# Performance work log

Hardware: AMD Instinct MI355X
Metric: run time of the kernel (lower is better)

The kernel has to match this reference:

```python
import jax, jax.numpy as jnp
import numpy as np

HIDDEN = 4096
LATENT = 32768


def setup_inputs() -> dict:
    key = jax.random.key(0)
    k1, k2, k3, k4, k5 = jax.random.split(key, 5)
    x = jax.random.normal(k1, (2, 2048, HIDDEN), dtype=jnp.float32)
    # learned params (loaded from checkpoint in the original; random here)
    pre_bias = jax.random.normal(k2, (HIDDEN,), dtype=jnp.float32) * 0.02
    latent_bias = jax.random.normal(k3, (LATENT,), dtype=jnp.float32) * 0.02
    # nn.Linear weights: encoder.weight [latent, hidden], decoder.weight [hidden, latent]
    enc_w = jax.random.normal(k4, (LATENT, HIDDEN), dtype=jnp.float32) / np.sqrt(HIDDEN)
    dec_w = jax.random.normal(k5, (HIDDEN, LATENT), dtype=jnp.float32) / np.sqrt(LATENT)
    return {"x": x, "pre_bias": pre_bias, "latent_bias": latent_bias,
            "enc_w": enc_w, "dec_w": dec_w, "k": 64}


def reference(x, pre_bias, latent_bias, enc_w, dec_w, k):
    B, S, H = x.shape
    L = enc_w.shape[0]
    # pre_acts = encoder(x - pre_bias) + latent_bias
    pre_acts = jnp.einsum('bsh,lh->bsl', x - pre_bias, enc_w) + latent_bias
    # TopK sparsification: keep top-k values per token, zero elsewhere
    flat = pre_acts.reshape(B * S, L)
    vals, idx = jax.lax.top_k(flat, k)                       # [N,k]
    rows = jnp.arange(B * S)[:, None]                        # [N,1]
    latents = jnp.zeros_like(flat).at[rows, idx].set(vals).reshape(B, S, L)
    # x_hat = decoder(latents) + pre_bias
    x_hat = jnp.einsum('bsl,hl->bsh', latents, dec_w) + pre_bias
    return latents, x_hat
```

## Files before the change

### kernel.cpp

```cpp
#include <hip/hip_runtime.h>
#include <hip/hip_fp16.h>

typedef unsigned short u16;
typedef unsigned int u32;
using f32x4 = __attribute__((ext_vector_type(4))) float;
using bf16x8 = __attribute__((ext_vector_type(8))) short;
using u32x4 = __attribute__((ext_vector_type(4))) u32;

#define M_TOK 4096
#define HID   4096
#define LAT   32768
#define TOPK  64

#define BM 128
#define BN 256
#define BK 32
#define NT (HID / BK)
#define LCAP 2048
#define CAND_T0 2.0f
#define WBAND 0.0625f

__device__ __forceinline__ u16 f2bf(float f) {
  u32 u = __builtin_bit_cast(u32, f);
  u32 r = 0x7fffu + ((u >> 16) & 1u);
  return (u16)((u + r) >> 16);
}

__global__ __launch_bounds__(256) void k_xs(const float* __restrict__ x,
                                            const float* __restrict__ pb,
                                            u16* __restrict__ xs) {
  size_t i = ((size_t)blockIdx.x * 256 + threadIdx.x) * 4;
  if (i >= (size_t)M_TOK * HID) return;
  float4 xv = *(const float4*)(x + i);
  float4 bv = *(const float4*)(pb + (i & (HID - 1)));
  ushort4 o;
  o.x = f2bf(xv.x - bv.x); o.y = f2bf(xv.y - bv.y);
  o.z = f2bf(xv.z - bv.z); o.w = f2bf(xv.w - bv.w);
  *(ushort4*)(xs + i) = o;
}

__global__ __launch_bounds__(256) void k_conv(const float* __restrict__ src,
                                              u16* __restrict__ dst, size_t n4) {
  size_t i = (size_t)blockIdx.x * 256 + threadIdx.x;
  size_t stride = (size_t)gridDim.x * 256;
  for (; i < n4; i += stride) {
    float4 v = ((const float4*)src)[i];
    ushort4 o;
    o.x = f2bf(v.x); o.y = f2bf(v.y); o.z = f2bf(v.z); o.w = f2bf(v.w);
    ((ushort4*)dst)[i] = o;
  }
}

__global__ __launch_bounds__(512, 4) void k_gemm(const u16* __restrict__ A,
                                                 const u16* __restrict__ B,
                                                 const float* __restrict__ lbias,
                                                 float2* __restrict__ lists,
                                                 int* __restrict__ cnt) {
  __shared__ __align__(16) u16 Asm[3][64][64];
  __shared__ __align__(16) u16 Bsm[3][128][64];
  const int tid = threadIdx.x;
  const int lane = tid & 63;
  const int wave = tid >> 6;
  const int wm = wave >> 2;
  const int wn = wave & 3;

  const int bid = blockIdx.x;
  const int wg = (bid & 7) * 512 + (bid >> 3);
  const int bm = (wg & 31) * BM;
  const int bn = (wg >> 5) * BN;

  const int sp = tid >> 3, sslot = tid & 7;
  const int ss0 = sslot ^ (sp & 7);
  const int sr = sp * 2 + (ss0 >> 2);
  const int sc = (ss0 & 3) << 3;
  const int sp2 = sp + 64;
  const int ss02 = sslot ^ (sp2 & 7);
  const int sr2 = sp2 * 2 + (ss02 >> 2);
  const int sc2 = (ss02 & 3) << 3;

  auto stage = [&](int t, int buf) {
    __builtin_amdgcn_global_load_lds(
        (const __attribute__((address_space(1))) void*)(
            A + (size_t)(bm + sr) * HID + t * BK + sc),
        (__attribute__((address_space(3))) void*)(&Asm[buf][sp][sslot << 3]), 16, 0, 0);
    __builtin_amdgcn_global_load_lds(
        (const __attribute__((address_space(1))) void*)(
            B + (size_t)(bn + sr) * HID + t * BK + sc),
        (__attribute__((address_space(3))) void*)(&Bsm[buf][sp][sslot << 3]), 16, 0, 0);
    __builtin_amdgcn_global_load_lds(
        (const __attribute__((address_space(1))) void*)(
            B + (size_t)(bn + sr2) * HID + t * BK + sc2),
        (__attribute__((address_space(3))) void*)(&Bsm[buf][sp2][sslot << 3]), 16, 0, 0);
  };

  const int chunk = lane >> 4;
  auto readA = [&](int buf, int m) -> bf16x8 {
    int r = wm * 64 + m * 16 + (lane & 15);
    int p = r >> 1;
    int s = (((r & 1) << 2) + chunk) ^ (p & 7);
    u32 off = (u32)(uintptr_t)(__attribute__((address_space(3))) const void*)(&Asm[buf][p][s << 3]);
    u32x4 rv;
    asm volatile("ds_read_b128 %0, %1" : "=v"(rv) : "v"(off));
    return __builtin_bit_cast(bf16x8, rv);
  };
  auto readB = [&](int buf, int n) -> bf16x8 {
    int r = wn * 64 + n * 16 + (lane & 15);
    int p = r >> 1;
    int s = (((r & 1) << 2) + chunk) ^ (p & 7);
    u32 off = (u32)(uintptr_t)(__attribute__((address_space(3))) const void*)(&Bsm[buf][p][s << 3]);
    u32x4 rv;
    asm volatile("ds_read_b128 %0, %1" : "=v"(rv) : "v"(off));
    return __builtin_bit_cast(bf16x8, rv);
  };

  f32x4 acc[4][4] = {};

#define BARRIER() asm volatile("s_barrier" ::: "memory")
#define LGKM0() do { asm volatile("s_waitcnt lgkmcnt(0)"); \
                     __builtin_amdgcn_sched_barrier(0); } while (0)
#define VMCNT3() asm volatile("s_waitcnt vmcnt(3)" ::: "memory")
#define VMCNT0() asm volatile("s_waitcnt vmcnt(0)" ::: "memory")

  stage(0, 0); stage(1, 1);
  VMCNT3();
  BARRIER();

#pragma unroll 1
  for (int t = 0; t < NT; ++t) {
    const int buf = t - (t / 3) * 3;
    if (t + 2 < NT) stage(t + 2, (t + 2) - ((t + 2) / 3) * 3);
    bf16x8 a[4], bb[4];
#pragma unroll
    for (int m = 0; m < 4; ++m) a[m] = readA(buf, m);
#pragma unroll
    for (int n = 0; n < 4; ++n) bb[n] = readB(buf, n);
    LGKM0();
    __builtin_amdgcn_s_setprio(1);
#pragma unroll
    for (int m = 0; m < 4; ++m)
#pragma unroll
      for (int n = 0; n < 4; ++n)
        acc[m][n] = __builtin_amdgcn_mfma_f32_16x16x32_bf16(a[m], bb[n], acc[m][n], 0, 0, 0);
    __builtin_amdgcn_s_setprio(0);
    if (t + 2 < NT) VMCNT3(); else VMCNT0();
    BARRIER();
  }

#pragma unroll
  for (int n = 0; n < 4; ++n) {
    int col = bn + wn * 64 + n * 16 + (lane & 15);
    float lb = lbias[col];
#pragma unroll
    for (int m = 0; m < 4; ++m) {
      int row = bm + wm * 64 + m * 16 + ((lane >> 4) << 2);
#pragma unroll
      for (int j = 0; j < 4; ++j) {
        float v = acc[m][n][j] + lb;
        if (v >= CAND_T0) {
          int p = atomicAdd(&cnt[row + j], 1);
          if (p < LCAP)
            lists[(size_t)(row + j) * LCAP + p] =
                make_float2(v, __builtin_bit_cast(float, col));
        }
      }
    }
  }
#undef BARRIER
#undef LGKM0
#undef VMCNT3
#undef VMCNT0
}

__global__ __launch_bounds__(256) void k_topk(
    const float2* __restrict__ lists, const int* __restrict__ cnt,
    const float* __restrict__ x,
    const float* __restrict__ pb,
    const float* __restrict__ enc_w,
    const float* __restrict__ lbias,
    int* __restrict__ oidx, float* __restrict__ oval) {
  const int row = blockIdx.x;
  const int tid = threadIdx.x;
  const int lane = tid & 63, wave = tid >> 6;

  __shared__ int cnum, innum, selnum;
  __shared__ float s_m;
  __shared__ int lidx[LCAP];
  __shared__ float laf[LCAP];
  __shared__ int cidx[352];
  __shared__ double cref[352];
  __shared__ int fidx[64];
  __shared__ float fval[64];

  const int n = min(cnt[row], LCAP);
  if (tid == 0) { s_m = -1e30f; cnum = 0; innum = 0; selnum = 0; }
  for (int j = tid; j < n; j += 256) {
    float2 e = lists[(size_t)row * LCAP + j];
    laf[j] = e.x;
    lidx[j] = __builtin_bit_cast(int, e.y);
  }
  __syncthreads();

  for (int j = tid; j < n; j += 256) {
    float aj = laf[j]; int ij = lidx[j];
    int rank = 0;
    for (int i2 = 0; i2 < n; ++i2) {
      float ai = laf[i2];
      rank += (ai > aj) || (ai == aj && lidx[i2] < ij);
    }
    if (rank == 63) s_m = aj;
  }
  __syncthreads();
  float mf = s_m;

  for (int j = tid; j < n; j += 256) {
    float aa = laf[j];
    if (aa > mf + WBAND) {
      int p = atomicAdd(&innum, 1);
      if (p < 64) { fidx[p] = lidx[j]; fval[p] = aa; }
    } else if (aa >= mf - WBAND) {
      int p = atomicAdd(&cnum, 1);
      if (p < 352) cidx[p] = lidx[j];
    }
  }
  __syncthreads();
  int nin = min(innum, 64);
  int nu = min(cnum, 352);

  const float* xrow = x + (size_t)row * HID;
  for (int cc = wave; cc < nu; cc += 4) {
    const float* wrow = enc_w + (size_t)cidx[cc] * HID;
    double s = 0.0;
    for (int i = lane * 4; i < HID; i += 256) {
      float4 wv = *(const float4*)(wrow + i);
      float4 xv = *(const float4*)(xrow + i);
      float4 bv = *(const float4*)(pb + i);
      s += ((double)xv.x - (double)bv.x) * (double)wv.x;
      s += ((double)xv.y - (double)bv.y) * (double)wv.y;
      s += ((double)xv.z - (double)bv.z) * (double)wv.z;
      s += ((double)xv.w - (double)bv.w) * (double)wv.w;
    }
#pragma unroll
    for (int off = 32; off > 0; off >>= 1) s += __shfl_down(s, off);
    if (lane == 0) cref[cc] = s + (double)lbias[cidx[cc]];
  }
  __syncthreads();

  int need = 64 - nin;
  for (int j = tid; j < nu; j += 256) {
    double rj = cref[j]; int ij = cidx[j];
    int rank = 0;
    for (int i2 = 0; i2 < nu; ++i2) {
      double ri = cref[i2];
      rank += (ri > rj) || (ri == rj && cidx[i2] < ij);
    }
    if (rank < need) {
      int p = atomicAdd(&selnum, 1);
      if (nin + p < 64) { fidx[nin + p] = ij; fval[nin + p] = (float)rj; }
    }
  }
  __syncthreads();

  if (tid < 64) {
    int my = fidx[tid]; float v = fval[tid];
    int rank = 0;
#pragma unroll
    for (int i2 = 0; i2 < 64; ++i2) rank += (fidx[i2] < my);
    oidx[row * 64 + rank] = my;
    oval[row * 64 + rank] = v;
  }
}

__global__ __launch_bounds__(256) void k_trans(const float* __restrict__ dw,
                                               u16* __restrict__ dt) {
  __shared__ float tile[64][65];
  int l0 = blockIdx.x * 64;
  int h0 = blockIdx.y * 64;
  int tx = threadIdx.x & 15;
  int ty = threadIdx.x >> 4;
#pragma unroll
  for (int i = 0; i < 4; ++i) {
    int r = ty + i * 16;
    float4 v = *(const float4*)(dw + (size_t)(h0 + r) * LAT + l0 + tx * 4);
    tile[r][tx * 4 + 0] = v.x; tile[r][tx * 4 + 1] = v.y;
    tile[r][tx * 4 + 2] = v.z; tile[r][tx * 4 + 3] = v.w;
  }
  __syncthreads();
#pragma unroll
  for (int i = 0; i < 4; ++i) {
    int r = ty + i * 16;
    ushort4 o;
    o.x = f2bf(tile[tx * 4 + 0][r]);
    o.y = f2bf(tile[tx * 4 + 1][r]);
    o.z = f2bf(tile[tx * 4 + 2][r]);
    o.w = f2bf(tile[tx * 4 + 3][r]);
    *(ushort4*)(dt + (size_t)(l0 + r) * HID + h0 + tx * 4) = o;
  }
}

__global__ __launch_bounds__(256) void k_decode(
    const int* __restrict__ oidx, const float* __restrict__ oval,
    const u16* __restrict__ dt, const float* __restrict__ pb,
    float* __restrict__ xh) {
  const int n = blockIdx.x, tid = threadIdx.x;
  __shared__ int sidx[64];
  __shared__ float sval[64];
  if (tid < 64) { sidx[tid] = oidx[n * 64 + tid]; sval[tid] = oval[n * 64 + tid]; }
  __syncthreads();
  const int h0 = tid * 16;
  float acc[16];
#pragma unroll
  for (int q = 0; q < 4; ++q) {
    float4 b = *(const float4*)(pb + h0 + q * 4);
    acc[q * 4 + 0] = b.x; acc[q * 4 + 1] = b.y;
    acc[q * 4 + 2] = b.z; acc[q * 4 + 3] = b.w;
  }
  for (int j = 0; j < 64; ++j) {
    float v = sval[j];
    const uint4* w = (const uint4*)(dt + (size_t)sidx[j] * HID + h0);
    uint4 p0 = w[0], p1 = w[1];
    u32 u[8] = {p0.x, p0.y, p0.z, p0.w, p1.x, p1.y, p1.z, p1.w};
#pragma unroll
    for (int q = 0; q < 8; ++q) {
      float lo = __builtin_bit_cast(float, u[q] << 16);
      float hi = __builtin_bit_cast(float, u[q] & 0xffff0000u);
      acc[q * 2 + 0] = fmaf(v, lo, acc[q * 2 + 0]);
      acc[q * 2 + 1] = fmaf(v, hi, acc[q * 2 + 1]);
    }
  }
#pragma unroll
  for (int q = 0; q < 4; ++q) {
    float4 o;
    o.x = acc[q * 4 + 0]; o.y = acc[q * 4 + 1];
    o.z = acc[q * 4 + 2]; o.w = acc[q * 4 + 3];
    *(float4*)(xh + (size_t)n * HID + h0 + q * 4) = o;
  }
}

__global__ __launch_bounds__(256) void k_lat(const int* __restrict__ oidx,
                                             const float* __restrict__ oval,
                                             float* __restrict__ lat) {
  const int n = blockIdx.x, tid = threadIdx.x;
  __shared__ int sidx[64];
  __shared__ float sval[64];
  if (tid < 64) { sidx[tid] = oidx[n * 64 + tid]; sval[tid] = oval[n * 64 + tid]; }
  float* row = lat + (size_t)n * LAT;
  float4 z = {0.f, 0.f, 0.f, 0.f};
  for (int q = tid; q < LAT / 4; q += 256) *(float4*)(row + q * 4) = z;
  __syncthreads();
  if (tid < 64) row[sidx[tid]] = sval[tid];
}

extern "C" void kernel_launch(void* const* d_in, const int* in_sizes, int n_in,
                              void* d_out, int out_size, void* d_ws, size_t ws_size,
                              hipStream_t stream) {
  const float* x = (const float*)d_in[0];
  const float* pre_bias = (const float*)d_in[1];
  const float* latent_bias = (const float*)d_in[2];
  const float* enc_w = (const float*)d_in[3];
  const float* dec_w = (const float*)d_in[4];

  float* latents = (float*)d_out;
  float* xhat = latents + (size_t)M_TOK * LAT;

  u16* xs = (u16*)xhat;
  u16* encb = (u16*)latents;
  float2* lists = (float2*)((char*)d_out + (size_t)M_TOK * LAT * 2);
  u16* decT = (u16*)latents;
  int* cnt = (int*)d_ws;
  int* oidx = (int*)((char*)d_ws + M_TOK * 4);
  float* oval = (float*)((char*)d_ws + M_TOK * 4 + (size_t)M_TOK * TOPK * 4);

  hipMemsetAsync(cnt, 0, M_TOK * 4, stream);
  k_xs<<<(M_TOK * HID / 4 + 255) / 256, 256, 0, stream>>>(x, pre_bias, xs);
  k_conv<<<4096, 256, 0, stream>>>(enc_w, encb, (size_t)LAT * HID / 4);
  k_gemm<<<(M_TOK / BM) * (LAT / BN), 512, 0, stream>>>(xs, encb, latent_bias, lists, cnt);
  k_topk<<<M_TOK, 256, 0, stream>>>(lists, cnt, x, pre_bias, enc_w, latent_bias, oidx, oval);
  k_trans<<<dim3(LAT / 64, HID / 64), 256, 0, stream>>>(dec_w, decT);
  k_decode<<<M_TOK, 256, 0, stream>>>(oidx, oval, decT, pre_bias, xhat);
  k_lat<<<M_TOK, 256, 0, stream>>>(oidx, oval, latents);
}
```

Measured before the change: 2.487 ms.

## Store transposed decoder weights in FP8 and fuse input conversion kernels

The decoder weight copy made by the transpose kernel is now stored as 8-bit floats scaled by 64, using hardware pack and unpack builtins where available and a software encoder otherwise. The decode kernel gathers half as many bytes per selected latent row, and the value scale is folded into the top-k values. The x-minus-bias conversion and the encoder weight bf16 conversion are merged into one grid-stride kernel, saving a launch. The top-k rescoring band (WBAND) is narrowed. FP8 weights lower decoder accuracy, and the narrower band may change which candidates get refined.

```diff
diff --git a/kernel.cpp b/kernel.cpp
--- a/kernel.cpp
+++ b/kernel.cpp
@@ -1,6 +1,7 @@
 #include <hip/hip_runtime.h>
 #include <hip/hip_fp16.h>
 
+typedef unsigned char u8;
 typedef unsigned short u16;
 typedef unsigned int u32;
 using f32x4 = __attribute__((ext_vector_type(4))) float;
@@ -18,7 +19,15 @@
 #define NT (HID / BK)
 #define LCAP 2048
 #define CAND_T0 2.0f
-#define WBAND 0.0625f
+#define WBAND 0.03f
+
+#if __has_builtin(__builtin_amdgcn_cvt_pk_f32_fp8) && __has_builtin(__builtin_amdgcn_cvt_pk_fp8_f32)
+#define HW_FP8 1
+#define VSCALE (1.0f / 64.0f)
+#else
+#define HW_FP8 0
+#define VSCALE 4.0f
+#endif
 
 __device__ __forceinline__ u16 f2bf(float f) {
   u32 u = __builtin_bit_cast(u32, f);
@@ -26,28 +35,43 @@
   return (u16)((u + r) >> 16);
 }
 
-__global__ __launch_bounds__(256) void k_xs(const float* __restrict__ x,
-                                            const float* __restrict__ pb,
-                                            u16* __restrict__ xs) {
-  size_t i = ((size_t)blockIdx.x * 256 + threadIdx.x) * 4;
-  if (i >= (size_t)M_TOK * HID) return;
-  float4 xv = *(const float4*)(x + i);
-  float4 bv = *(const float4*)(pb + (i & (HID - 1)));
-  ushort4 o;
-  o.x = f2bf(xv.x - bv.x); o.y = f2bf(xv.y - bv.y);
-  o.z = f2bf(xv.z - bv.z); o.w = f2bf(xv.w - bv.w);
-  *(ushort4*)(xs + i) = o;
-}
-
-__global__ __launch_bounds__(256) void k_conv(const float* __restrict__ src,
-                                              u16* __restrict__ dst, size_t n4) {
+#if !HW_FP8
+__device__ __forceinline__ u8 enc_fp8(float w) {
+  _Float16 hf = (_Float16)(w * 64.0f);
+  u16 h = __builtin_bit_cast(u16, hf);
+  u16 s = (h >> 8) & 0x80;
+  u16 mag = h & 0x7fff;
+  if (mag < 0x2400) return (u8)s;
+  int eman = ((int)mag + 0x40 - 0x2000) >> 7;
+  if (eman > 0x7e) eman = 0x7e;
+  return (u8)(s | eman);
+}
+__device__ __forceinline__ float dec_fp8(u32 b) {
+  u16 h = (u16)(((b & 0x80u) << 8) | ((b & 0x7fu) << 7));
+  return (float)__builtin_bit_cast(_Float16, h);
+}
+#endif
+
+__global__ __launch_bounds__(256) void k_convx(const float* __restrict__ x,
+                                               const float* __restrict__ pb,
+                                               u16* __restrict__ xs,
+                                               const float* __restrict__ ew,
+                                               u16* __restrict__ encb) {
+  const size_t stride = (size_t)gridDim.x * 256;
   size_t i = (size_t)blockIdx.x * 256 + threadIdx.x;
-  size_t stride = (size_t)gridDim.x * 256;
-  for (; i < n4; i += stride) {
-    float4 v = ((const float4*)src)[i];
+  for (size_t q = i; q < (size_t)M_TOK * HID / 4; q += stride) {
+    float4 xv = ((const float4*)x)[q];
+    float4 bv = *(const float4*)(pb + ((q * 4) & (HID - 1)));
+    ushort4 o;
+    o.x = f2bf(xv.x - bv.x); o.y = f2bf(xv.y - bv.y);
+    o.z = f2bf(xv.z - bv.z); o.w = f2bf(xv.w - bv.w);
+    ((ushort4*)xs)[q] = o;
+  }
+  for (size_t q = i; q < (size_t)LAT * HID / 4; q += stride) {
+    float4 v = ((const float4*)ew)[q];
     ushort4 o;
     o.x = f2bf(v.x); o.y = f2bf(v.y); o.z = f2bf(v.z); o.w = f2bf(v.w);
-    ((ushort4*)dst)[i] = o;
+    ((ushort4*)encb)[q] = o;
   }
 }
 
@@ -271,7 +295,7 @@
 }
 
 __global__ __launch_bounds__(256) void k_trans(const float* __restrict__ dw,
-                                               u16* __restrict__ dt) {
+                                               u8* __restrict__ dt) {
   __shared__ float tile[64][65];
   int l0 = blockIdx.x * 64;
   int h0 = blockIdx.y * 64;
@@ -288,23 +312,31 @@
 #pragma unroll
   for (int i = 0; i < 4; ++i) {
     int r = ty + i * 16;
-    ushort4 o;
-    o.x = f2bf(tile[tx * 4 + 0][r]);
-    o.y = f2bf(tile[tx * 4 + 1][r]);
-    o.z = f2bf(tile[tx * 4 + 2][r]);
-    o.w = f2bf(tile[tx * 4 + 3][r]);
-    *(ushort4*)(dt + (size_t)(l0 + r) * HID + h0 + tx * 4) = o;
+    float a = tile[tx * 4 + 0][r], b = tile[tx * 4 + 1][r];
+    float c = tile[tx * 4 + 2][r], d = tile[tx * 4 + 3][r];
+#if HW_FP8
+    int pk = __builtin_amdgcn_cvt_pk_fp8_f32(a * 64.0f, b * 64.0f, 0, false);
+    pk = __builtin_amdgcn_cvt_pk_fp8_f32(c * 64.0f, d * 64.0f, pk, true);
+    *(u32*)(dt + (size_t)(l0 + r) * HID + h0 + tx * 4) = (u32)pk;
+#else
+    u32 pk = (u32)enc_fp8(a) | ((u32)enc_fp8(b) << 8) |
+             ((u32)enc_fp8(c) << 16) | ((u32)enc_fp8(d) << 24);
+    *(u32*)(dt + (size_t)(l0 + r) * HID + h0 + tx * 4) = pk;
+#endif
   }
 }
 
 __global__ __launch_bounds__(256) void k_decode(
     const int* __restrict__ oidx, const float* __restrict__ oval,
-    const u16* __restrict__ dt, const float* __restrict__ pb,
+    const u8* __restrict__ dt, const float* __restrict__ pb,
     float* __restrict__ xh) {
   const int n = blockIdx.x, tid = threadIdx.x;
   __shared__ int sidx[64];
   __shared__ float sval[64];
-  if (tid < 64) { sidx[tid] = oidx[n * 64 + tid]; sval[tid] = oval[n * 64 + tid]; }
+  if (tid < 64) {
+    sidx[tid] = oidx[n * 64 + tid];
+    sval[tid] = oval[n * 64 + tid] * VSCALE;
+  }
   __syncthreads();
   const int h0 = tid * 16;
   float acc[16];
@@ -316,15 +348,23 @@
   }
   for (int j = 0; j < 64; ++j) {
     float v = sval[j];
-    const uint4* w = (const uint4*)(dt + (size_t)sidx[j] * HID + h0);
-    uint4 p0 = w[0], p1 = w[1];
-    u32 u[8] = {p0.x, p0.y, p0.z, p0.w, p1.x, p1.y, p1.z, p1.w};
-#pragma unroll
-    for (int q = 0; q < 8; ++q) {
-      float lo = __builtin_bit_cast(float, u[q] << 16);
-      float hi = __builtin_bit_cast(float, u[q] & 0xffff0000u);
-      acc[q * 2 + 0] = fmaf(v, lo, acc[q * 2 + 0]);
-      acc[q * 2 + 1] = fmaf(v, hi, acc[q * 2 + 1]);
+    uint4 p = *(const uint4*)(dt + (size_t)sidx[j] * HID + h0);
+    u32 u[4] = {p.x, p.y, p.z, p.w};
+#pragma unroll
+    for (int q = 0; q < 4; ++q) {
+#if HW_FP8
+      auto lo = __builtin_amdgcn_cvt_pk_f32_fp8(u[q], false);
+      auto hi = __builtin_amdgcn_cvt_pk_f32_fp8(u[q], true);
+      acc[q * 4 + 0] = fmaf(v, lo[0], acc[q * 4 + 0]);
+      acc[q * 4 + 1] = fmaf(v, lo[1], acc[q * 4 + 1]);
+      acc[q * 4 + 2] = fmaf(v, hi[0], acc[q * 4 + 2]);
+      acc[q * 4 + 3] = fmaf(v, hi[1], acc[q * 4 + 3]);
+#else
+      acc[q * 4 + 0] = fmaf(v, dec_fp8(u[q] & 0xffu), acc[q * 4 + 0]);
+      acc[q * 4 + 1] = fmaf(v, dec_fp8((u[q] >> 8) & 0xffu), acc[q * 4 + 1]);
+      acc[q * 4 + 2] = fmaf(v, dec_fp8((u[q] >> 16) & 0xffu), acc[q * 4 + 2]);
+      acc[q * 4 + 3] = fmaf(v, dec_fp8(u[q] >> 24), acc[q * 4 + 3]);
+#endif
     }
   }
 #pragma unroll
@@ -365,14 +405,13 @@
   u16* xs = (u16*)xhat;
   u16* encb = (u16*)latents;
   float2* lists = (float2*)((char*)d_out + (size_t)M_TOK * LAT * 2);
-  u16* decT = (u16*)latents;
+  u8* decT = (u8*)latents;
   int* cnt = (int*)d_ws;
   int* oidx = (int*)((char*)d_ws + M_TOK * 4);
   float* oval = (float*)((char*)d_ws + M_TOK * 4 + (size_t)M_TOK * TOPK * 4);
 
   hipMemsetAsync(cnt, 0, M_TOK * 4, stream);
-  k_xs<<<(M_TOK * HID / 4 + 255) / 256, 256, 0, stream>>>(x, pre_bias, xs);
-  k_conv<<<4096, 256, 0, stream>>>(enc_w, encb, (size_t)LAT * HID / 4);
+  k_convx<<<4096, 256, 0, stream>>>(x, pre_bias, xs, enc_w, encb);
   k_gemm<<<(M_TOK / BM) * (LAT / BN), 512, 0, stream>>>(xs, encb, latent_bias, lists, cnt);
   k_topk<<<M_TOK, 256, 0, stream>>>(lists, cnt, x, pre_bias, enc_w, latent_bias, oidx, oval);
   k_trans<<<dim3(LAT / 64, HID / 64), 256, 0, stream>>>(dec_w, decT);
```

Result: faster. 2.183 ms (-12.2%).
